# Kernel tuning notes

Hardware: AMD Instinct MI355X
Metric: run time of the kernel (lower is better)

Reference implementation:

```python
import jax, jax.numpy as jnp
import numpy as np

RHO = 1.0
LAMBD = 0.1
ALPHA = 0.5
N_IT = 20
MIN_VALUE = 1e-40
EPSILON = 1e-10


def setup_inputs() -> dict:
    key = jax.random.key(0)
    R_0 = jax.random.uniform(key, (16, 1024, 1024), dtype=jnp.float32)
    return {"R_0": R_0}


def _compute_R(R_0, X, Z):
    R_0 = jnp.where(R_0 == 0, MIN_VALUE, R_0)
    X = jnp.where(X == 0, MIN_VALUE, X)
    tmp = (jnp.log(R_0) + RHO * jnp.log(X) - Z) / (1.0 + RHO)
    return jax.nn.softmax(tmp, axis=2)


def _compute_X(R, Z):
    # vectorized over the column loop: group soft-thresholding per column i
    x = R + Z / RHO                              # [B, M, N]
    threshold = ALPHA * LAMBD / RHO
    s_td = jnp.sign(x) * jnp.maximum(jnp.abs(x) - threshold, 0.0)
    # torch.norm over the full [B, M] slice -> scalar per column i
    col_norm = jnp.sqrt(jnp.sum(s_td * s_td, axis=(0, 1)))  # [N]
    scale = jnp.maximum(1.0 - (1.0 - ALPHA) * LAMBD / (RHO * col_norm + EPSILON), 0.0)
    return scale[None, None, :] * s_td


def _compute_Z(Z, R, X):
    return Z + RHO * (R - X)


def reference(R_0):
    def step(carry, _):
        R, X, Z = carry
        R = _compute_R(R_0, X, Z)
        X = _compute_X(R, Z)
        Z = _compute_Z(Z, R, X)
        return (R, X, Z), None

    Z0 = jnp.zeros_like(R_0)
    (R, X, Z), _ = jax.lax.scan(step, (R_0, R_0, Z0), None, length=N_IT)
    return R
```

## Files before the change

### kernel.cpp

```cpp
#include <hip/hip_runtime.h>
#include <math.h>

#define NN 1024
#define NROWS 16384
#define TPB 256
#define WPB 4
#define KSLOT 16
#define NIT 20

#define F_RPW 8
#define F_RPB (WPB * F_RPW)
#define F_NGRID (NROWS / F_RPB)

#define FB_RPW 2
#define FB_RPB (WPB * FB_RPW)
#define FB_NGRID (NROWS / FB_RPB)

#define MINV 1e-40f
#define THR  0.05f
#define SCLC 0.05f
#define EPSL 1e-10f

#define CS_BYTES ((size_t)NIT * KSLOT * NN * sizeof(float))
#define NARR 64
#define ARR_STRIDE 16
#define BLKS_PER_ARR (F_NGRID / NARR)

__device__ __forceinline__ float wred_sum(float v) {
#pragma unroll
  for (int o = 32; o > 0; o >>= 1) v += __shfl_xor(v, o, 64);
  return v;
}
__device__ __forceinline__ float softthr_full(float x) {
  return copysignf(fmaxf(fabsf(x) - THR, 0.0f), x);
}

__device__ __forceinline__ void gbar2(unsigned* __restrict__ arr,
                                      unsigned* __restrict__ rel, unsigned g) {
  __syncthreads();
  if (threadIdx.x == 0) {
    __threadfence();
    __hip_atomic_fetch_add(&arr[(blockIdx.x & (NARR - 1)) * ARR_STRIDE], 1u,
                           __ATOMIC_RELEASE, __HIP_MEMORY_SCOPE_AGENT);
  }
  if (blockIdx.x == 0) {
    if (threadIdx.x < NARR) {
      const unsigned tgt = (unsigned)BLKS_PER_ARR * g;
      while (__hip_atomic_load(&arr[threadIdx.x * ARR_STRIDE], __ATOMIC_RELAXED,
                               __HIP_MEMORY_SCOPE_AGENT) < tgt)
        __builtin_amdgcn_s_sleep(1);
    }
    __syncthreads();
    if (threadIdx.x == 0) {
      __threadfence();
      __hip_atomic_store(rel, g, __ATOMIC_RELEASE, __HIP_MEMORY_SCOPE_AGENT);
    }
  } else {
    if (threadIdx.x == 0) {
      while (__hip_atomic_load(rel, __ATOMIC_RELAXED,
                               __HIP_MEMORY_SCOPE_AGENT) < g)
        __builtin_amdgcn_s_sleep(2);
      __threadfence();
    }
    __syncthreads();
  }
}

__global__ __launch_bounds__(TPB, 2) void k_fused(const float* __restrict__ R0,
                                                  float* __restrict__ OUT,
                                                  float* __restrict__ SQ,
                                                  float* __restrict__ cs,
                                                  unsigned* __restrict__ arr,
                                                  unsigned* __restrict__ rel) {
  __shared__ float s_scale[NN];
  __shared__ float s_part[WPB * NN];
  const int lane = threadIdx.x & 63;
  const int wv = threadIdx.x >> 6;
  const size_t row0 = (size_t)blockIdx.x * F_RPB + (size_t)wv * F_RPW;

  float V[F_RPW][16];

#pragma unroll
  for (int rr = 0; rr < F_RPW; ++rr) {
    const size_t base = (row0 + rr) * NN + (size_t)lane * 4;
    float sloc = 0.f;
#pragma unroll
    for (int c = 0; c < 4; ++c) {
      const float4 r4 = *(const float4*)(R0 + base + c * 256);
      const float p0 = (r4.x == 0.f) ? MINV : r4.x;
      const float p1 = (r4.y == 0.f) ? MINV : r4.y;
      const float p2 = (r4.z == 0.f) ? MINV : r4.z;
      const float p3 = (r4.w == 0.f) ? MINV : r4.w;
      V[rr][c * 4 + 0] = p0;
      V[rr][c * 4 + 1] = p1;
      V[rr][c * 4 + 2] = p2;
      V[rr][c * 4 + 3] = p3;
      sloc += (p0 + p1) + (p2 + p3);
      *(float4*)(SQ + base + c * 256) =
          make_float4(sqrtf(p0), sqrtf(p1), sqrtf(p2), sqrtf(p3));
    }
    const float inv = 1.0f / wred_sum(sloc);
#pragma unroll
    for (int c = 0; c < 4; ++c) {
      float a[4];
#pragma unroll
      for (int j = 0; j < 4; ++j) {
        const float rn = V[rr][c * 4 + j] * inv;
        V[rr][c * 4 + j] = rn;
        const float s = fmaxf(rn - THR, 0.f);
        a[j] = s * s;
      }
      float* sp = &s_part[wv * NN + c * 256 + lane * 4];
      if (rr == 0) {
        *(float4*)sp = make_float4(a[0], a[1], a[2], a[3]);
      } else {
        float4 o = *(float4*)sp;
        *(float4*)sp = make_float4(o.x + a[0], o.y + a[1], o.z + a[2], o.w + a[3]);
      }
    }
  }
  __syncthreads();
  {
    const int col = threadIdx.x * 4;
    const float4 s0 = *(float4*)(&s_part[0 * NN + col]);
    const float4 s1 = *(float4*)(&s_part[1 * NN + col]);
    const float4 s2 = *(float4*)(&s_part[2 * NN + col]);
    const float4 s3 = *(float4*)(&s_part[3 * NN + col]);
    float* dst = cs + (size_t)(blockIdx.x & (KSLOT - 1)) * NN + col;
    atomicAdd(dst + 0, (s0.x + s1.x) + (s2.x + s3.x));
    atomicAdd(dst + 1, (s0.y + s1.y) + (s2.y + s3.y));
    atomicAdd(dst + 2, (s0.z + s1.z) + (s2.z + s3.z));
    atomicAdd(dst + 3, (s0.w + s1.w) + (s2.w + s3.w));
  }
  gbar2(arr, rel, 1u);

#pragma unroll 1
  for (int t = 1; t < NIT; ++t) {
    const int last = (t == NIT - 1) ? 1 : 0;
    const float* csP = cs + (size_t)(t - 1) * KSLOT * NN;
    float* csN = cs + (size_t)t * KSLOT * NN;

    {
      const int col = threadIdx.x * 4;
      float4 a = make_float4(0.f, 0.f, 0.f, 0.f);
#pragma unroll
      for (int k = 0; k < KSLOT; ++k) {
        const float4 v = *(const float4*)(csP + (size_t)k * NN + col);
        a.x += v.x; a.y += v.y; a.z += v.z; a.w += v.w;
      }
      s_scale[col + 0] = fmaxf(1.0f - SCLC / (sqrtf(a.x) + EPSL), 0.0f);
      s_scale[col + 1] = fmaxf(1.0f - SCLC / (sqrtf(a.y) + EPSL), 0.0f);
      s_scale[col + 2] = fmaxf(1.0f - SCLC / (sqrtf(a.z) + EPSL), 0.0f);
      s_scale[col + 3] = fmaxf(1.0f - SCLC / (sqrtf(a.w) + EPSL), 0.0f);
    }
    __syncthreads();

#pragma unroll
    for (int rr = 0; rr < F_RPW; ++rr) {
      const size_t base = (row0 + rr) * NN + (size_t)lane * 4;
      float u[16];
      float sloc = 0.f;
#pragma unroll
      for (int c = 0; c < 4; ++c) {
        const float4 sq4 = *(const float4*)(SQ + base + c * 256);
        const float4 sc4 = *(const float4*)(&s_scale[c * 256 + lane * 4]);
        const float sq[4] = {sq4.x, sq4.y, sq4.z, sq4.w};
        const float sc[4] = {sc4.x, sc4.y, sc4.z, sc4.w};
#pragma unroll
        for (int j = 0; j < 4; ++j) {
          const float vv = V[rr][c * 4 + j];
          const float s = fmaxf(vv - THR, 0.f);
          const float X = sc[j] * s;
          const float zz = vv - X;
          const float Xm = (X == 0.f) ? MINV : X;
          const float uu = sq[j] * sqrtf(Xm) * __expf(-0.5f * zz);
          u[c * 4 + j] = uu;
          V[rr][c * 4 + j] = zz;
          sloc += uu;
        }
      }
      const float inv = 1.0f / wred_sum(sloc);
      if (!last) {
#pragma unroll
        for (int c = 0; c < 4; ++c) {
          float a[4];
#pragma unroll
          for (int j = 0; j < 4; ++j) {
            const float nv = u[c * 4 + j] * inv + V[rr][c * 4 + j];
            V[rr][c * 4 + j] = nv;
            const float s = fmaxf(nv - THR, 0.f);
            a[j] = s * s;
          }
          float* sp = &s_part[wv * NN + c * 256 + lane * 4];
          if (rr == 0) {
            *(float4*)sp = make_float4(a[0], a[1], a[2], a[3]);
          } else {
            float4 o = *(float4*)sp;
            *(float4*)sp =
                make_float4(o.x + a[0], o.y + a[1], o.z + a[2], o.w + a[3]);
          }
        }
      } else {
#pragma unroll
        for (int c = 0; c < 4; ++c) {
          *(float4*)(OUT + base + c * 256) =
              make_float4(u[c * 4 + 0] * inv, u[c * 4 + 1] * inv,
                          u[c * 4 + 2] * inv, u[c * 4 + 3] * inv);
        }
      }
    }

    if (!last) {
      __syncthreads();
      {
        const int col = threadIdx.x * 4;
        const float4 s0 = *(float4*)(&s_part[0 * NN + col]);
        const float4 s1 = *(float4*)(&s_part[1 * NN + col]);
        const float4 s2 = *(float4*)(&s_part[2 * NN + col]);
        const float4 s3 = *(float4*)(&s_part[3 * NN + col]);
        float* dst = csN + (size_t)(blockIdx.x & (KSLOT - 1)) * NN + col;
        atomicAdd(dst + 0, (s0.x + s1.x) + (s2.x + s3.x));
        atomicAdd(dst + 1, (s0.y + s1.y) + (s2.y + s3.y));
        atomicAdd(dst + 2, (s0.z + s1.z) + (s2.z + s3.z));
        atomicAdd(dst + 3, (s0.w + s1.w) + (s2.w + s3.w));
      }
      gbar2(arr, rel, (unsigned)(t + 1));
    }
  }
}

__global__ __launch_bounds__(TPB) void k_start(const float* __restrict__ R0,
                                               float* __restrict__ V,
                                               float* __restrict__ SQ,
                                               float* __restrict__ cs0) {
  __shared__ float s_part[WPB * NN];
  const int lane = threadIdx.x & 63;
  const int wv = threadIdx.x >> 6;
#pragma unroll
  for (int rr = 0; rr < FB_RPW; ++rr) {
    const size_t row = (size_t)blockIdx.x * FB_RPB + wv * FB_RPW + rr;
    const size_t base = row * NN + (size_t)lane * 4;
    float r0v[16];
    float sloc = 0.f;
#pragma unroll
    for (int c = 0; c < 4; ++c) {
      const float4 r4 = *(const float4*)(R0 + base + c * 256);
      r0v[c * 4 + 0] = (r4.x == 0.f) ? MINV : r4.x;
      r0v[c * 4 + 1] = (r4.y == 0.f) ? MINV : r4.y;
      r0v[c * 4 + 2] = (r4.z == 0.f) ? MINV : r4.z;
      r0v[c * 4 + 3] = (r4.w == 0.f) ? MINV : r4.w;
      sloc += (r0v[c * 4 + 0] + r0v[c * 4 + 1]) + (r0v[c * 4 + 2] + r0v[c * 4 + 3]);
      *(float4*)(SQ + base + c * 256) =
          make_float4(sqrtf(r0v[c * 4 + 0]), sqrtf(r0v[c * 4 + 1]),
                      sqrtf(r0v[c * 4 + 2]), sqrtf(r0v[c * 4 + 3]));
    }
    const float inv = 1.0f / wred_sum(sloc);
#pragma unroll
    for (int c = 0; c < 4; ++c) {
      float rn[4], a[4];
#pragma unroll
      for (int j = 0; j < 4; ++j) {
        rn[j] = r0v[c * 4 + j] * inv;
        const float s = softthr_full(rn[j]);
        a[j] = s * s;
      }
      *(float4*)(V + base + c * 256) = make_float4(rn[0], rn[1], rn[2], rn[3]);
      float* sp = &s_part[wv * NN + c * 256 + lane * 4];
      if (rr == 0) {
        *(float4*)sp = make_float4(a[0], a[1], a[2], a[3]);
      } else {
        float4 o = *(float4*)sp;
        *(float4*)sp = make_float4(o.x + a[0], o.y + a[1], o.z + a[2], o.w + a[3]);
      }
    }
  }
  __syncthreads();
  const int col = threadIdx.x * 4;
  const float4 s0 = *(float4*)(&s_part[0 * NN + col]);
  const float4 s1 = *(float4*)(&s_part[1 * NN + col]);
  const float4 s2 = *(float4*)(&s_part[2 * NN + col]);
  const float4 s3 = *(float4*)(&s_part[3 * NN + col]);
  float* dst = cs0 + (size_t)(blockIdx.x & (KSLOT - 1)) * NN + col;
  atomicAdd(dst + 0, (s0.x + s1.x) + (s2.x + s3.x));
  atomicAdd(dst + 1, (s0.y + s1.y) + (s2.y + s3.y));
  atomicAdd(dst + 2, (s0.z + s1.z) + (s2.z + s3.z));
  atomicAdd(dst + 3, (s0.w + s1.w) + (s2.w + s3.w));
}

__global__ __launch_bounds__(TPB) void k_ab(float* __restrict__ V,
                                            const float* __restrict__ SQ,
                                            const float* __restrict__ csPrev,
                                            float* __restrict__ csNext,
                                            int last) {
  __shared__ float s_scale[NN];
  __shared__ float s_part[WPB * NN];
  const int lane = threadIdx.x & 63;
  const int wv = threadIdx.x >> 6;
  {
    const int col = threadIdx.x * 4;
    float4 a = make_float4(0.f, 0.f, 0.f, 0.f);
#pragma unroll
    for (int k = 0; k < KSLOT; ++k) {
      const float4 v = *(const float4*)(csPrev + (size_t)k * NN + col);
      a.x += v.x; a.y += v.y; a.z += v.z; a.w += v.w;
    }
    s_scale[col + 0] = fmaxf(1.0f - SCLC / (sqrtf(a.x) + EPSL), 0.0f);
    s_scale[col + 1] = fmaxf(1.0f - SCLC / (sqrtf(a.y) + EPSL), 0.0f);
    s_scale[col + 2] = fmaxf(1.0f - SCLC / (sqrtf(a.z) + EPSL), 0.0f);
    s_scale[col + 3] = fmaxf(1.0f - SCLC / (sqrtf(a.w) + EPSL), 0.0f);
  }
  __syncthreads();

#pragma unroll
  for (int rr = 0; rr < FB_RPW; ++rr) {
    const size_t row = (size_t)blockIdx.x * FB_RPB + wv * FB_RPW + rr;
    const size_t base = row * NN + (size_t)lane * 4;
    float u[16], z[16];
    float sloc = 0.f;
#pragma unroll
    for (int c = 0; c < 4; ++c) {
      const float4 vv4 = *(const float4*)(V + base + c * 256);
      const float4 sq4 = *(const float4*)(SQ + base + c * 256);
      const float4 sc4 = *(const float4*)(&s_scale[c * 256 + lane * 4]);
      const float vv[4] = {vv4.x, vv4.y, vv4.z, vv4.w};
      const float sq[4] = {sq4.x, sq4.y, sq4.z, sq4.w};
      const float sc[4] = {sc4.x, sc4.y, sc4.z, sc4.w};
#pragma unroll
      for (int j = 0; j < 4; ++j) {
        const float s = softthr_full(vv[j]);
        const float X = sc[j] * s;
        const float zz = vv[j] - X;
        z[c * 4 + j] = zz;
        const float Xm = (X == 0.f) ? MINV : X;
        const float uu = sq[j] * sqrtf(Xm) * __expf(-0.5f * zz);
        u[c * 4 + j] = uu;
        sloc += uu;
      }
    }
    const float inv = 1.0f / wred_sum(sloc);
#pragma unroll
    for (int c = 0; c < 4; ++c) {
      float outv[4];
#pragma unroll
      for (int j = 0; j < 4; ++j) {
        const float rn = u[c * 4 + j] * inv;
        outv[j] = last ? rn : (rn + z[c * 4 + j]);
      }
      *(float4*)(V + base + c * 256) =
          make_float4(outv[0], outv[1], outv[2], outv[3]);
      if (!last) {
        float a[4];
#pragma unroll
        for (int j = 0; j < 4; ++j) {
          const float s = softthr_full(outv[j]);
          a[j] = s * s;
        }
        float* sp = &s_part[wv * NN + c * 256 + lane * 4];
        if (rr == 0) {
          *(float4*)sp = make_float4(a[0], a[1], a[2], a[3]);
        } else {
          float4 o = *(float4*)sp;
          *(float4*)sp =
              make_float4(o.x + a[0], o.y + a[1], o.z + a[2], o.w + a[3]);
        }
      }
    }
  }
  if (!last) {
    __syncthreads();
    const int col = threadIdx.x * 4;
    const float4 s0 = *(float4*)(&s_part[0 * NN + col]);
    const float4 s1 = *(float4*)(&s_part[1 * NN + col]);
    const float4 s2 = *(float4*)(&s_part[2 * NN + col]);
    const float4 s3 = *(float4*)(&s_part[3 * NN + col]);
    float* dst = csNext + (size_t)(blockIdx.x & (KSLOT - 1)) * NN + col;
    atomicAdd(dst + 0, (s0.x + s1.x) + (s2.x + s3.x));
    atomicAdd(dst + 1, (s0.y + s1.y) + (s2.y + s3.y));
    atomicAdd(dst + 2, (s0.z + s1.z) + (s2.z + s3.z));
    atomicAdd(dst + 3, (s0.w + s1.w) + (s2.w + s3.w));
  }
}

extern "C" void kernel_launch(void* const* d_in, const int* in_sizes, int n_in,
                              void* d_out, int out_size, void* d_ws, size_t ws_size,
                              hipStream_t stream) {
  (void)in_sizes; (void)n_in; (void)out_size; (void)ws_size;
  const float* R0 = (const float*)d_in[0];
  float* OUT = (float*)d_out;
  float* SQ = (float*)d_ws;
  float* cs = (float*)((char*)d_ws + (size_t)NROWS * NN * sizeof(float));
  unsigned* arr = (unsigned*)((char*)cs + CS_BYTES);
  unsigned* rel = arr + NARR * ARR_STRIDE + 64;

  static int mode = -1;
  if (mode < 0) {
    mode = 0;
    int dev = 0, ncu = 0;
    if (hipGetDevice(&dev) == hipSuccess &&
        hipDeviceGetAttribute(&ncu, hipDeviceAttributeMultiprocessorCount,
                              dev) == hipSuccess) {
      if (2L * (long)ncu >= (long)F_NGRID) mode = 1;
    }
  }

  hipMemsetAsync(cs, 0, CS_BYTES + 8192, stream);
  if (mode == 1) {
    k_fused<<<F_NGRID, TPB, 0, stream>>>(R0, OUT, SQ, cs, arr, rel);
  } else {
    k_start<<<FB_NGRID, TPB, 0, stream>>>(R0, OUT, SQ, cs);
    for (int it = 1; it < NIT; ++it) {
      k_ab<<<FB_NGRID, TPB, 0, stream>>>(OUT, SQ,
                                         cs + (size_t)(it - 1) * KSLOT * NN,
                                         cs + (size_t)it * KSLOT * NN,
                                         (it == NIT - 1) ? 1 : 0);
    }
  }
}
```

Measured before the change: 1.027 ms.

## Keep sqrt(R0) in LDS as fp16 and accumulate column norms in registers

The persistent fused kernel used to write sqrt(R0) to global memory and re-read it every iteration. It now stores those values as fp16 in LDS, so the per-iteration loop no longer touches global memory except for the small column-sum buffers. Per-thread column partial sums are accumulated in registers and reduced through LDS atomics. The number of global atomic slots drops from 16 to 8. This adds fp16 rounding error on the sqrt term and needs about 68KB of dynamic LDS per block, which could limit the two-blocks-per-CU residency the grid barrier relies on.

Measured after the change: 883.9 us. 1.16x faster.

```diff
diff --git a/kernel.cpp b/kernel.cpp
--- a/kernel.cpp
+++ b/kernel.cpp
@@ -1,20 +1,23 @@
 #include <hip/hip_runtime.h>
+#include <hip/hip_fp16.h>
 #include <math.h>
 
 #define NN 1024
 #define NROWS 16384
 #define TPB 256
 #define WPB 4
-#define KSLOT 16
 #define NIT 20
 
 #define F_RPW 8
 #define F_RPB (WPB * F_RPW)
 #define F_NGRID (NROWS / F_RPB)
+#define F_KSLOT 8
+#define F_LDS_BYTES (32 * NN * 2 + NN * 4)
 
 #define FB_RPW 2
 #define FB_RPB (WPB * FB_RPW)
 #define FB_NGRID (NROWS / FB_RPB)
+#define KSLOT 16
 
 #define MINV 1e-40f
 #define THR  0.05f
@@ -25,6 +28,8 @@
 #define NARR 64
 #define ARR_STRIDE 16
 #define BLKS_PER_ARR (F_NGRID / NARR)
+
+struct h4 { __half2 a, b; };
 
 __device__ __forceinline__ float wred_sum(float v) {
 #pragma unroll
@@ -66,19 +71,52 @@
   }
 }
 
+__device__ __forceinline__ void reduce_push(float* __restrict__ s_red,
+                                            float (&csloc)[16],
+                                            float* __restrict__ dstbase,
+                                            int wv, int lane) {
+  __syncthreads();
+  if (wv == 0) {
+#pragma unroll
+    for (int c = 0; c < 4; ++c)
+      *(float4*)(&s_red[c * 256 + lane * 4]) = make_float4(
+          csloc[c * 4 + 0], csloc[c * 4 + 1], csloc[c * 4 + 2], csloc[c * 4 + 3]);
+  }
+  __syncthreads();
+  if (wv != 0) {
+#pragma unroll
+    for (int c = 0; c < 4; ++c) {
+#pragma unroll
+      for (int j = 0; j < 4; ++j)
+        atomicAdd(&s_red[c * 256 + lane * 4 + j], csloc[c * 4 + j]);
+    }
+  }
+  __syncthreads();
+  const int col = (wv * 64 + lane) * 4;
+  const float4 v = *(const float4*)(&s_red[col]);
+  atomicAdd(dstbase + col + 0, v.x);
+  atomicAdd(dstbase + col + 1, v.y);
+  atomicAdd(dstbase + col + 2, v.z);
+  atomicAdd(dstbase + col + 3, v.w);
+}
+
 __global__ __launch_bounds__(TPB, 2) void k_fused(const float* __restrict__ R0,
                                                   float* __restrict__ OUT,
-                                                  float* __restrict__ SQ,
                                                   float* __restrict__ cs,
                                                   unsigned* __restrict__ arr,
                                                   unsigned* __restrict__ rel) {
-  __shared__ float s_scale[NN];
-  __shared__ float s_part[WPB * NN];
+  extern __shared__ char smem[];
+  __half* sq_h = (__half*)smem;
+  float* s_red = (float*)(smem + 32 * NN * 2);
   const int lane = threadIdx.x & 63;
   const int wv = threadIdx.x >> 6;
-  const size_t row0 = (size_t)blockIdx.x * F_RPB + (size_t)wv * F_RPW;
+  const int lrow = wv * F_RPW;
+  const size_t row0 = (size_t)blockIdx.x * F_RPB + lrow;
 
   float V[F_RPW][16];
+  float csloc[16];
+#pragma unroll
+  for (int i = 0; i < 16; ++i) csloc[i] = 0.f;
 
 #pragma unroll
   for (int rr = 0; rr < F_RPW; ++rr) {
@@ -96,84 +134,79 @@
       V[rr][c * 4 + 2] = p2;
       V[rr][c * 4 + 3] = p3;
       sloc += (p0 + p1) + (p2 + p3);
-      *(float4*)(SQ + base + c * 256) =
-          make_float4(sqrtf(p0), sqrtf(p1), sqrtf(p2), sqrtf(p3));
+      h4 hv;
+      hv.a = __floats2half2_rn(sqrtf(p0), sqrtf(p1));
+      hv.b = __floats2half2_rn(sqrtf(p2), sqrtf(p3));
+      *(h4*)(&sq_h[(lrow + rr) * NN + c * 256 + lane * 4]) = hv;
     }
     const float inv = 1.0f / wred_sum(sloc);
 #pragma unroll
     for (int c = 0; c < 4; ++c) {
-      float a[4];
 #pragma unroll
       for (int j = 0; j < 4; ++j) {
         const float rn = V[rr][c * 4 + j] * inv;
         V[rr][c * 4 + j] = rn;
         const float s = fmaxf(rn - THR, 0.f);
-        a[j] = s * s;
-      }
-      float* sp = &s_part[wv * NN + c * 256 + lane * 4];
-      if (rr == 0) {
-        *(float4*)sp = make_float4(a[0], a[1], a[2], a[3]);
-      } else {
-        float4 o = *(float4*)sp;
-        *(float4*)sp = make_float4(o.x + a[0], o.y + a[1], o.z + a[2], o.w + a[3]);
-      }
-    }
-  }
-  __syncthreads();
-  {
-    const int col = threadIdx.x * 4;
-    const float4 s0 = *(float4*)(&s_part[0 * NN + col]);
-    const float4 s1 = *(float4*)(&s_part[1 * NN + col]);
-    const float4 s2 = *(float4*)(&s_part[2 * NN + col]);
-    const float4 s3 = *(float4*)(&s_part[3 * NN + col]);
-    float* dst = cs + (size_t)(blockIdx.x & (KSLOT - 1)) * NN + col;
-    atomicAdd(dst + 0, (s0.x + s1.x) + (s2.x + s3.x));
-    atomicAdd(dst + 1, (s0.y + s1.y) + (s2.y + s3.y));
-    atomicAdd(dst + 2, (s0.z + s1.z) + (s2.z + s3.z));
-    atomicAdd(dst + 3, (s0.w + s1.w) + (s2.w + s3.w));
-  }
+        csloc[c * 4 + j] += s * s;
+      }
+    }
+  }
+  reduce_push(s_red, csloc, cs + (size_t)(blockIdx.x & (F_KSLOT - 1)) * NN,
+              wv, lane);
   gbar2(arr, rel, 1u);
 
 #pragma unroll 1
   for (int t = 1; t < NIT; ++t) {
     const int last = (t == NIT - 1) ? 1 : 0;
-    const float* csP = cs + (size_t)(t - 1) * KSLOT * NN;
-    float* csN = cs + (size_t)t * KSLOT * NN;
+    const float* csP = cs + (size_t)(t - 1) * F_KSLOT * NN;
+    float* csN = cs + (size_t)t * F_KSLOT * NN;
 
     {
       const int col = threadIdx.x * 4;
       float4 a = make_float4(0.f, 0.f, 0.f, 0.f);
 #pragma unroll
-      for (int k = 0; k < KSLOT; ++k) {
+      for (int k = 0; k < F_KSLOT; ++k) {
         const float4 v = *(const float4*)(csP + (size_t)k * NN + col);
         a.x += v.x; a.y += v.y; a.z += v.z; a.w += v.w;
       }
-      s_scale[col + 0] = fmaxf(1.0f - SCLC / (sqrtf(a.x) + EPSL), 0.0f);
-      s_scale[col + 1] = fmaxf(1.0f - SCLC / (sqrtf(a.y) + EPSL), 0.0f);
-      s_scale[col + 2] = fmaxf(1.0f - SCLC / (sqrtf(a.z) + EPSL), 0.0f);
-      s_scale[col + 3] = fmaxf(1.0f - SCLC / (sqrtf(a.w) + EPSL), 0.0f);
+      float4 sc4;
+      sc4.x = fmaxf(1.0f - SCLC / (sqrtf(a.x) + EPSL), 0.0f);
+      sc4.y = fmaxf(1.0f - SCLC / (sqrtf(a.y) + EPSL), 0.0f);
+      sc4.z = fmaxf(1.0f - SCLC / (sqrtf(a.z) + EPSL), 0.0f);
+      sc4.w = fmaxf(1.0f - SCLC / (sqrtf(a.w) + EPSL), 0.0f);
+      *(float4*)(&s_red[col]) = sc4;
     }
     __syncthreads();
 
+    float scr[16];
+#pragma unroll
+    for (int c = 0; c < 4; ++c) {
+      const float4 s4 = *(const float4*)(&s_red[c * 256 + lane * 4]);
+      scr[c * 4 + 0] = s4.x; scr[c * 4 + 1] = s4.y;
+      scr[c * 4 + 2] = s4.z; scr[c * 4 + 3] = s4.w;
+    }
+#pragma unroll
+    for (int i = 0; i < 16; ++i) csloc[i] = 0.f;
+
 #pragma unroll
     for (int rr = 0; rr < F_RPW; ++rr) {
-      const size_t base = (row0 + rr) * NN + (size_t)lane * 4;
       float u[16];
       float sloc = 0.f;
 #pragma unroll
       for (int c = 0; c < 4; ++c) {
-        const float4 sq4 = *(const float4*)(SQ + base + c * 256);
-        const float4 sc4 = *(const float4*)(&s_scale[c * 256 + lane * 4]);
-        const float sq[4] = {sq4.x, sq4.y, sq4.z, sq4.w};
-        const float sc[4] = {sc4.x, sc4.y, sc4.z, sc4.w};
+        const h4 hv =
+            *(const h4*)(&sq_h[(lrow + rr) * NN + c * 256 + lane * 4]);
+        const float2 f01 = __half22float2(hv.a);
+        const float2 f23 = __half22float2(hv.b);
+        const float sqv[4] = {f01.x, f01.y, f23.x, f23.y};
 #pragma unroll
         for (int j = 0; j < 4; ++j) {
           const float vv = V[rr][c * 4 + j];
           const float s = fmaxf(vv - THR, 0.f);
-          const float X = sc[j] * s;
+          const float X = scr[c * 4 + j] * s;
           const float zz = vv - X;
           const float Xm = (X == 0.f) ? MINV : X;
-          const float uu = sq[j] * sqrtf(Xm) * __expf(-0.5f * zz);
+          const float uu = sqv[j] * sqrtf(Xm) * __expf(-0.5f * zz);
           u[c * 4 + j] = uu;
           V[rr][c * 4 + j] = zz;
           sloc += uu;
@@ -183,24 +216,16 @@
       if (!last) {
 #pragma unroll
         for (int c = 0; c < 4; ++c) {
-          float a[4];
 #pragma unroll
           for (int j = 0; j < 4; ++j) {
             const float nv = u[c * 4 + j] * inv + V[rr][c * 4 + j];
             V[rr][c * 4 + j] = nv;
             const float s = fmaxf(nv - THR, 0.f);
-            a[j] = s * s;
-          }
-          float* sp = &s_part[wv * NN + c * 256 + lane * 4];
-          if (rr == 0) {
-            *(float4*)sp = make_float4(a[0], a[1], a[2], a[3]);
-          } else {
-            float4 o = *(float4*)sp;
-            *(float4*)sp =
-                make_float4(o.x + a[0], o.y + a[1], o.z + a[2], o.w + a[3]);
+            csloc[c * 4 + j] += s * s;
           }
         }
       } else {
+        const size_t base = (row0 + rr) * NN + (size_t)lane * 4;
 #pragma unroll
         for (int c = 0; c < 4; ++c) {
           *(float4*)(OUT + base + c * 256) =
@@ -211,19 +236,8 @@
     }
 
     if (!last) {
-      __syncthreads();
-      {
-        const int col = threadIdx.x * 4;
-        const float4 s0 = *(float4*)(&s_part[0 * NN + col]);
-        const float4 s1 = *(float4*)(&s_part[1 * NN + col]);
-        const float4 s2 = *(float4*)(&s_part[2 * NN + col]);
-        const float4 s3 = *(float4*)(&s_part[3 * NN + col]);
-        float* dst = csN + (size_t)(blockIdx.x & (KSLOT - 1)) * NN + col;
-        atomicAdd(dst + 0, (s0.x + s1.x) + (s2.x + s3.x));
-        atomicAdd(dst + 1, (s0.y + s1.y) + (s2.y + s3.y));
-        atomicAdd(dst + 2, (s0.z + s1.z) + (s2.z + s3.z));
-        atomicAdd(dst + 3, (s0.w + s1.w) + (s2.w + s3.w));
-      }
+      reduce_push(s_red, csloc,
+                  csN + (size_t)(blockIdx.x & (F_KSLOT - 1)) * NN, wv, lane);
       gbar2(arr, rel, (unsigned)(t + 1));
     }
   }
@@ -398,14 +412,18 @@
     int dev = 0, ncu = 0;
     if (hipGetDevice(&dev) == hipSuccess &&
         hipDeviceGetAttribute(&ncu, hipDeviceAttributeMultiprocessorCount,
-                              dev) == hipSuccess) {
-      if (2L * (long)ncu >= (long)F_NGRID) mode = 1;
+                              dev) == hipSuccess &&
+        2L * (long)ncu >= (long)F_NGRID &&
+        hipFuncSetAttribute(reinterpret_cast<const void*>(k_fused),
+                            hipFuncAttributeMaxDynamicSharedMemorySize,
+                            F_LDS_BYTES) == hipSuccess) {
+      mode = 1;
     }
   }
 
   hipMemsetAsync(cs, 0, CS_BYTES + 8192, stream);
   if (mode == 1) {
-    k_fused<<<F_NGRID, TPB, 0, stream>>>(R0, OUT, SQ, cs, arr, rel);
+    k_fused<<<F_NGRID, TPB, F_LDS_BYTES, stream>>>(R0, OUT, cs, arr, rel);
   } else {
     k_start<<<FB_NGRID, TPB, 0, stream>>>(R0, OUT, SQ, cs);
     for (int it = 1; it < NIT; ++it) {
```
